# Optimization experiments

Measured on AMD Instinct MI355X. Metric: run time of the kernel, lower is better.

The kernel has to match this reference:

```python
import jax, jax.numpy as jnp
import numpy as np

B, S, D, H = 4, 1024, 1024, 16
DH = D // H
K_SPARSE = 32
LAMBDA_MAX, ALPHA = 10.0, 5.0
SPARSE_THRESHOLD = 1.0


def setup_inputs() -> dict:
    key = jax.random.key(0)
    ks = jax.random.split(key, 12)
    x = jax.random.normal(ks[0], (B, S, D), dtype=jnp.float32)
    prior_mask = jax.random.bernoulli(ks[1], 0.1, (S, S))
    prior_indices = jax.random.randint(ks[2], (S, K_SPARSE), 0, S)
    prior_index_mask = jax.random.bernoulli(ks[3], 0.9, (S, K_SPARSE))
    prior_index_mask = prior_index_mask.at[:, 0].set(True)  # avoid all-masked rows
    u_prev = jax.random.normal(ks[4], (B, 1), dtype=jnp.float32)
    sc = 1.0 / np.sqrt(D)
    Wq = jax.random.normal(ks[5], (D, D), dtype=jnp.float32) * sc
    Wk = jax.random.normal(ks[6], (D, D), dtype=jnp.float32) * sc
    Wv = jax.random.normal(ks[7], (D, D), dtype=jnp.float32) * sc
    Wo = jax.random.normal(ks[8], (D, D), dtype=jnp.float32) * sc
    bq = jnp.zeros((D,), jnp.float32)
    bk = jnp.zeros((D,), jnp.float32)
    bv = jnp.zeros((D,), jnp.float32)
    bo = jnp.zeros((D,), jnp.float32)
    return {"x": x, "prior_mask": prior_mask, "prior_indices": prior_indices,
            "prior_index_mask": prior_index_mask, "u_prev": u_prev,
            "Wq": Wq, "bq": bq, "Wk": Wk, "bk": bk, "Wv": Wv, "bv": bv,
            "Wo": Wo, "bo": bo}


def reference(x, prior_mask, prior_indices, prior_index_mask, u_prev,
              Wq, bq, Wk, bk, Wv, bv, Wo, bo):
    Bb, Ss, Dd = x.shape
    scale = 1.0 / jnp.sqrt(jnp.asarray(DH, x.dtype))

    def proj(W, b):
        return (x @ W.T + b).reshape(Bb, Ss, H, DH).transpose(0, 2, 1, 3)  # [B,H,S,DH]

    Q, K, V = proj(Wq, bq), proj(Wk, bk), proj(Wv, bv)

    lam = LAMBDA_MAX * jnp.exp(-ALPHA * u_prev.reshape(Bb))  # [B]
    use_sparse = lam >= SPARSE_THRESHOLD                      # [B] bool

    # ---- dense branch: full SDPA with lambda-scaled prior bias ----
    scores = jnp.einsum('bhqd,bhkd->bhqk', Q, K) * scale      # [B,H,S,S]
    prior_bias = jnp.where(prior_mask[:Ss, :Ss], 0.0, -1.0).astype(x.dtype)
    bias = lam[:, None, None, None] * prior_bias[None, None]
    dense_out = jnp.einsum('bhqk,bhkd->bhqd',
                           jax.nn.softmax(scores + bias, axis=-1), V)

    # ---- sparse branch: gather-indexed SDPA over prior_indices ----
    idx = prior_indices[:Ss]                                   # [S,k]
    Kg = K[:, :, idx]                                          # [B,H,S,k,DH]
    Vg = V[:, :, idx]
    s_scores = jnp.einsum('bhsd,bhskd->bhsk', Q, Kg) * scale   # [B,H,S,k]
    s_scores = jnp.where(prior_index_mask[:Ss][None, None], s_scores,
                         jnp.asarray(-jnp.inf, x.dtype))
    sparse_out = jnp.einsum('bhsk,bhskd->bhsd',
                            jax.nn.softmax(s_scores, axis=-1), Vg)

    out = jnp.where(use_sparse[:, None, None, None], sparse_out, dense_out)
    out = out.transpose(0, 2, 1, 3).reshape(Bb, Ss, Dd)
    return out @ Wo.T + bo
```

## Files before the change

kernel.cpp:

```cpp
#include <hip/hip_runtime.h>
#include <hip/hip_bf16.h>
#include <cmath>

#define NB 4
#define NS 1024
#define ND 1024
#define NH 16
#define NDH 64
#define NKSP 32
#define SCALE 0.125f

typedef __attribute__((ext_vector_type(8))) short bf16x8;
typedef __attribute__((ext_vector_type(4))) float f32x4;
typedef unsigned long long u64;

#define AS1 __attribute__((address_space(1)))
#define AS3 __attribute__((address_space(3)))

__device__ __forceinline__ void gl_lds16(const void* g, void* l) {
    __builtin_amdgcn_global_load_lds((const AS1 void*)g, (AS3 void*)l, 16, 0, 0);
}

__device__ __forceinline__ ushort f2bf(float f) {
    union { __hip_bfloat16 h; ushort u; } cv;
    cv.h = __float2bfloat16(f);
    return cv.u;
}
__device__ __forceinline__ float bf2f(ushort u) {
    union { unsigned int i; float f; } cv;
    cv.i = ((unsigned int)u) << 16;
    return cv.f;
}

__global__ __launch_bounds__(256)
void f2bf_multi(const float* __restrict__ x,
                const float* __restrict__ w0, const float* __restrict__ w1,
                const float* __restrict__ w2, const float* __restrict__ w3,
                const int* __restrict__ pm,
                ushort* __restrict__ xo,
                ushort* __restrict__ o0, ushort* __restrict__ o1,
                ushort* __restrict__ o2, ushort* __restrict__ o3,
                u64* __restrict__ bm)
{
    int y = blockIdx.y;
    if (y == 5) {
        int word = blockIdx.x * 4 + (threadIdx.x >> 6);
        int lane = threadIdx.x & 63;
        int row  = word >> 4, wcol = word & 15;
        int v = pm[(size_t)row * NS + wcol * 64 + lane];
        u64 b = __ballot(v != 0);
        if (lane == 0) bm[word] = b;
        return;
    }
    const float* src; ushort* dst; int nblk;
    if (y == 0)      { src = x;  dst = xo; nblk = 4096; }
    else if (y == 1) { src = w0; dst = o0; nblk = 1024; }
    else if (y == 2) { src = w1; dst = o1; nblk = 1024; }
    else if (y == 3) { src = w2; dst = o2; nblk = 1024; }
    else             { src = w3; dst = o3; nblk = 1024; }
    if (blockIdx.x >= (unsigned)nblk) return;
    int i = (blockIdx.x * 256 + threadIdx.x) * 4;
    float4 v = *(const float4*)&src[i];
    ushort4 o;
    o.x = f2bf(v.x); o.y = f2bf(v.y); o.z = f2bf(v.z); o.w = f2bf(v.w);
    *(ushort4*)&dst[i] = o;
}

__global__ __launch_bounds__(256)
void gemm_qkv(const ushort* __restrict__ xb,
              const ushort* __restrict__ Wqb, const ushort* __restrict__ Wkb,
              const ushort* __restrict__ Wvb,
              const float* __restrict__ bq, const float* __restrict__ bk,
              const float* __restrict__ bv,
              ushort* __restrict__ Qo, ushort* __restrict__ Ko,
              ushort* __restrict__ Vo, ushort* __restrict__ Vto)
{
    constexpr int K = ND;
    __shared__ __attribute__((aligned(16))) ushort As[128 * 32];
    __shared__ __attribute__((aligned(16))) ushort Bs[128 * 32];

    const int tid  = threadIdx.x;
    const int lane = tid & 63, w = tid >> 6;
    const int wm = w >> 1, wn = w & 1;
    const int which = blockIdx.x >> 3;
    const int n0 = (blockIdx.x & 7) * 128;
    const int m0 = blockIdx.y * 128;
    const int quad = lane >> 4, l16 = lane & 15;

    const ushort* W = (which == 0) ? Wqb : (which == 1) ? Wkb : Wvb;
    const float* bias = (which == 0) ? bq : (which == 1) ? bk : bv;
    ushort* Out = (which == 0) ? Qo : (which == 1) ? Ko : Vo;

    f32x4 acc[4][4] = {};

    for (int k0 = 0; k0 < K; k0 += 32) {
        __syncthreads();
#pragma unroll
        for (int u = 0; u < 2; ++u) {
            int t0 = u * 256 + w * 64;
            int t  = t0 + lane;
            int row = t >> 2, kc = (t & 3) * 8;
            gl_lds16(xb + (size_t)(m0 + row) * K + k0 + kc, &As[t0 * 8]);
            gl_lds16(W  + (size_t)(n0 + row) * K + k0 + kc, &Bs[t0 * 8]);
        }
        __syncthreads();

        bf16x8 af[4], bfr[4];
#pragma unroll
        for (int mt = 0; mt < 4; ++mt)
            af[mt] = *(const bf16x8*)&As[(wm*64 + mt*16 + l16) * 32 + quad*8];
#pragma unroll
        for (int nt = 0; nt < 4; ++nt)
            bfr[nt] = *(const bf16x8*)&Bs[(wn*64 + nt*16 + l16) * 32 + quad*8];
#pragma unroll
        for (int mt = 0; mt < 4; ++mt)
#pragma unroll
            for (int nt = 0; nt < 4; ++nt)
                acc[mt][nt] = __builtin_amdgcn_mfma_f32_16x16x32_bf16(
                    af[mt], bfr[nt], acc[mt][nt], 0, 0, 0);
    }

#pragma unroll
    for (int nt = 0; nt < 4; ++nt) {
        int n = n0 + wn*64 + nt*16 + l16;
        float bz = bias[n];
        int hh = n >> 6, dh = n & 63;
#pragma unroll
        for (int mt = 0; mt < 4; ++mt) {
#pragma unroll
            for (int rg = 0; rg < 4; ++rg) {
                int m = m0 + wm*64 + mt*16 + quad*4 + rg;
                int b = m >> 10, s = m & (NS - 1);
                ushort val = f2bf(acc[mt][nt][rg] + bz);
                Out[(((size_t)(b*NH + hh))*NS + s)*NDH + dh] = val;
                if (which == 2)
                    Vto[(((size_t)(b*NH + hh))*NDH + dh)*NS + s] = val;
            }
        }
    }
}

__global__ __launch_bounds__(256)
void gemm_out(const ushort* __restrict__ A, const ushort* __restrict__ W,
              const float* __restrict__ bias, float* __restrict__ Cout)
{
    constexpr int K = ND;
    __shared__ __attribute__((aligned(16))) ushort As[64 * 32];
    __shared__ __attribute__((aligned(16))) ushort Bs[128 * 32];

    const int tid  = threadIdx.x;
    const int lane = tid & 63, w = tid >> 6;
    const int wm = w & 1, wn = w >> 1;
    const int m0 = blockIdx.y * 64, n0 = blockIdx.x * 128;
    const int quad = lane >> 4, l16 = lane & 15;

    f32x4 acc[2][4] = {};

    for (int k0 = 0; k0 < K; k0 += 32) {
        __syncthreads();
        {
            int t0 = w * 64;
            int t  = t0 + lane;
            int row = t >> 2, kc = (t & 3) * 8;
            gl_lds16(A + (size_t)(m0 + row) * K + k0 + kc, &As[t0 * 8]);
        }
#pragma unroll
        for (int u = 0; u < 2; ++u) {
            int t0 = u * 256 + w * 64;
            int t  = t0 + lane;
            int row = t >> 2, kc = (t & 3) * 8;
            gl_lds16(W + (size_t)(n0 + row) * K + k0 + kc, &Bs[t0 * 8]);
        }
        __syncthreads();

        bf16x8 af[2], bfr[4];
#pragma unroll
        for (int mt = 0; mt < 2; ++mt)
            af[mt] = *(const bf16x8*)&As[(wm*32 + mt*16 + l16) * 32 + quad*8];
#pragma unroll
        for (int nt = 0; nt < 4; ++nt)
            bfr[nt] = *(const bf16x8*)&Bs[(wn*64 + nt*16 + l16) * 32 + quad*8];
#pragma unroll
        for (int mt = 0; mt < 2; ++mt)
#pragma unroll
            for (int nt = 0; nt < 4; ++nt)
                acc[mt][nt] = __builtin_amdgcn_mfma_f32_16x16x32_bf16(
                    af[mt], bfr[nt], acc[mt][nt], 0, 0, 0);
    }

#pragma unroll
    for (int nt = 0; nt < 4; ++nt) {
        int n = n0 + wn*64 + nt*16 + l16;
        float bz = bias[n];
#pragma unroll
        for (int mt = 0; mt < 2; ++mt) {
#pragma unroll
            for (int rg = 0; rg < 4; ++rg) {
                int m = m0 + wm*32 + mt*16 + quad*4 + rg;
                Cout[(size_t)m * ND + n] = acc[mt][nt][rg] + bz;
            }
        }
    }
}

__global__ __launch_bounds__(256)
void attn_kernel(const ushort* __restrict__ Qb, const ushort* __restrict__ Kb,
                 const ushort* __restrict__ Vb, const ushort* __restrict__ Vt,
                 const u64* __restrict__ bm,
                 const int* __restrict__ pidx, const int* __restrict__ pimask,
                 const float* __restrict__ u_prev, ushort* __restrict__ OA)
{
    __shared__ __attribute__((aligned(16))) ushort Ks[64 * 72];
    __shared__ __attribute__((aligned(16))) ushort Vts[64 * 72];
    __shared__ __attribute__((aligned(16))) ushort Ps[128 * 68];
    __shared__ __attribute__((aligned(16))) u64    MW[128 * 16];

    const int tid  = threadIdx.x;
    const int lane = tid & 63, w = tid >> 6;
    const int quad = lane >> 4, l16 = lane & 15;

    const int id    = blockIdx.x;
    const int xcd   = id & 7;
    const int seq   = id >> 3;
    const int head  = xcd * 8 + (seq >> 3);
    const int qtile = seq & 7;
    const int b = head >> 4, h = head & 15;
    const int s0 = qtile * 128;

    const float lam = 10.0f * __expf(-5.0f * u_prev[b]);
    const bool sparse = (lam >= 1.0f);

    const size_t bh = (size_t)b * NH + h;
    const ushort* Qh  = Qb + bh * NS * NDH;
    const ushort* Kh  = Kb + bh * NS * NDH;
    const ushort* Vh  = Vb + bh * NS * NDH;
    const ushort* Vth = Vt + bh * NDH * NS;

    if (!sparse) {
#pragma unroll
        for (int u = 0; u < 8; ++u) {
            int idx = u * 256 + tid;
            MW[idx] = bm[(size_t)s0 * 16 + idx];
        }

        bf16x8 qf[2][2];
#pragma unroll
        for (int qh = 0; qh < 2; ++qh)
#pragma unroll
            for (int kk = 0; kk < 2; ++kk)
                qf[qh][kk] = *(const bf16x8*)
                    &Qh[(size_t)(s0 + w*32 + qh*16 + l16) * NDH + kk*32 + quad*8];

        union { bf16x8 v; ushort s[8]; } ones;
#pragma unroll
        for (int i = 0; i < 8; ++i) ones.s[i] = 0x3F80;

        f32x4 o_acc[2][4] = {};
        f32x4 l_acc[2] = {};

        const int sl = tid >> 2, c0 = (tid & 3) * 16;

        bf16x8 kreg[2], vreg[2];
        {
            const ushort* ksrc = &Kh[(size_t)sl * NDH + c0];
            kreg[0] = *(const bf16x8*)ksrc;
            kreg[1] = *(const bf16x8*)(ksrc + 8);
            const ushort* vsrc = &Vth[(size_t)sl * NS + c0];
            vreg[0] = *(const bf16x8*)vsrc;
            vreg[1] = *(const bf16x8*)(vsrc + 8);
        }

        for (int kt = 0; kt < 16; ++kt) {
            __syncthreads();
            *(bf16x8*)&Ks[sl*72 + c0]      = kreg[0];
            *(bf16x8*)&Ks[sl*72 + c0 + 8]  = kreg[1];
            *(bf16x8*)&Vts[sl*72 + c0]     = vreg[0];
            *(bf16x8*)&Vts[sl*72 + c0 + 8] = vreg[1];
            __syncthreads();

            if (kt < 15) {
                const ushort* ksrc = &Kh[(size_t)((kt+1)*64 + sl) * NDH + c0];
                kreg[0] = *(const bf16x8*)ksrc;
                kreg[1] = *(const bf16x8*)(ksrc + 8);
                const ushort* vsrc = &Vth[(size_t)sl * NS + (kt+1)*64 + c0];
                vreg[0] = *(const bf16x8*)vsrc;
                vreg[1] = *(const bf16x8*)(vsrc + 8);
            }

#pragma unroll
            for (int qh = 0; qh < 2; ++qh) {
                f32x4 s_acc[4] = {};
#pragma unroll
                for (int nt = 0; nt < 4; ++nt)
#pragma unroll
                    for (int kk = 0; kk < 2; ++kk) {
                        bf16x8 kf = *(const bf16x8*)&Ks[(nt*16 + l16)*72 + kk*32 + quad*8];
                        s_acc[nt] = __builtin_amdgcn_mfma_f32_16x16x32_bf16(
                            qf[qh][kk], kf, s_acc[nt], 0, 0, 0);
                    }

                u64 wv[4];
#pragma unroll
                for (int rg = 0; rg < 4; ++rg)
                    wv[rg] = MW[(w*32 + qh*16 + quad*4 + rg) * 16 + kt];
#pragma unroll
                for (int nt = 0; nt < 4; ++nt)
#pragma unroll
                    for (int rg = 0; rg < 4; ++rg) {
                        float bias = ((wv[rg] >> (nt*16 + l16)) & 1ULL) ? 0.f : -lam;
                        float p = __expf(fmaf(s_acc[nt][rg], SCALE, bias));
                        Ps[(w*32 + qh*16 + quad*4 + rg) * 68 + nt*16 + l16] = f2bf(p);
                    }

                bf16x8 pf[2];
#pragma unroll
                for (int kk = 0; kk < 2; ++kk)
                    pf[kk] = *(const bf16x8*)&Ps[(w*32 + qh*16 + l16)*68 + kk*32 + quad*8];
#pragma unroll
                for (int kk = 0; kk < 2; ++kk) {
                    l_acc[qh] = __builtin_amdgcn_mfma_f32_16x16x32_bf16(
                        pf[kk], ones.v, l_acc[qh], 0, 0, 0);
#pragma unroll
                    for (int nt = 0; nt < 4; ++nt) {
                        bf16x8 vf = *(const bf16x8*)&Vts[(nt*16 + l16)*72 + kk*32 + quad*8];
                        o_acc[qh][nt] = __builtin_amdgcn_mfma_f32_16x16x32_bf16(
                            pf[kk], vf, o_acc[qh][nt], 0, 0, 0);
                    }
                }
            }
        }

#pragma unroll
        for (int qh = 0; qh < 2; ++qh) {
            float inv[4];
#pragma unroll
            for (int rg = 0; rg < 4; ++rg) inv[rg] = 1.f / l_acc[qh][rg];
#pragma unroll
            for (int nt = 0; nt < 4; ++nt)
#pragma unroll
                for (int rg = 0; rg < 4; ++rg) {
                    int m = w*32 + qh*16 + quad*4 + rg;
                    OA[((size_t)b*NS + s0 + m)*ND + h*NDH + nt*16 + l16] =
                        f2bf(o_acc[qh][nt][rg] * inv[rg]);
                }
        }
    } else {
        const int r   = lane & 15;
        const int cg  = lane >> 4;
#pragma unroll
        for (int qh = 0; qh < 2; ++qh) {
            const int row = w*32 + qh*16 + r;

            float qreg[64];
            {
                const ushort* qp = Qh + (size_t)(s0 + row) * NDH;
#pragma unroll
                for (int c = 0; c < 8; ++c) {
                    union { bf16x8 v; ushort s[8]; } qv;
                    qv.v = *(const bf16x8*)(qp + c*8);
#pragma unroll
                    for (int j = 0; j < 8; ++j) qreg[c*8 + j] = bf2f(qv.s[j]);
                }
            }

            float sc[8];
#pragma unroll
            for (int jj = 0; jj < 8; ++jj) {
                int j  = cg*8 + jj;
                int mv = pimask[(size_t)(s0+row)*NKSP + j];
                if (mv) {
                    int kv = pidx[(size_t)(s0+row)*NKSP + j];
                    const ushort* krow = &Kh[(size_t)kv * NDH];
                    float acc = 0.f;
#pragma unroll
                    for (int c = 0; c < 8; ++c) {
                        union { bf16x8 v; ushort s[8]; } kk;
                        kk.v = *(const bf16x8*)(krow + c*8);
#pragma unroll
                        for (int jb = 0; jb < 8; ++jb)
                            acc = fmaf(qreg[c*8 + jb], bf2f(kk.s[jb]), acc);
                    }
                    sc[jj] = acc * SCALE;
                } else {
                    sc[jj] = -INFINITY;
                }
            }
            float mt = sc[0];
#pragma unroll
            for (int jj = 1; jj < 8; ++jj) mt = fmaxf(mt, sc[jj]);
            mt = fmaxf(mt, __shfl_xor(mt, 16));
            mt = fmaxf(mt, __shfl_xor(mt, 32));

            float psum = 0.f;
#pragma unroll
            for (int jj = 0; jj < 8; ++jj) {
                float p = __expf(sc[jj] - mt);
                psum += p;
                Ps[row * 68 + cg*8 + jj] = f2bf(p);
            }
            psum += __shfl_xor(psum, 16);
            psum += __shfl_xor(psum, 32);

            float o[16];
#pragma unroll
            for (int i = 0; i < 16; ++i) o[i] = 0.f;

            for (int j = 0; j < 32; ++j) {
                float p = bf2f(Ps[row * 68 + j]);
                if (p != 0.f) {
                    int kv = pidx[(size_t)(s0+row)*NKSP + j];
                    const ushort* vrow = &Vh[(size_t)kv * NDH + cg*16];
#pragma unroll
                    for (int c = 0; c < 2; ++c) {
                        union { bf16x8 v; ushort s[8]; } vv;
                        vv.v = *(const bf16x8*)(vrow + c*8);
#pragma unroll
                        for (int jb = 0; jb < 8; ++jb)
                            o[c*8 + jb] = fmaf(p, bf2f(vv.s[jb]), o[c*8 + jb]);
                    }
                }
            }

            float inv = 1.f / psum;
            ushort* op = OA + ((size_t)b*NS + s0 + row)*ND + h*NDH + cg*16;
#pragma unroll
            for (int i4 = 0; i4 < 4; ++i4) {
                ushort4 v;
                v.x = f2bf(o[i4*4+0]*inv); v.y = f2bf(o[i4*4+1]*inv);
                v.z = f2bf(o[i4*4+2]*inv); v.w = f2bf(o[i4*4+3]*inv);
                *(ushort4*)(op + i4*4) = v;
            }
        }
    }
}

extern "C" void kernel_launch(void* const* d_in, const int* in_sizes, int n_in,
                              void* d_out, int out_size, void* d_ws, size_t ws_size,
                              hipStream_t stream)
{
    const float* x      = (const float*)d_in[0];
    const int*   pmask  = (const int*)  d_in[1];
    const int*   pidx   = (const int*)  d_in[2];
    const int*   pimask = (const int*)  d_in[3];
    const float* u_prev = (const float*)d_in[4];
    const float* Wq     = (const float*)d_in[5];
    const float* bq     = (const float*)d_in[6];
    const float* Wk     = (const float*)d_in[7];
    const float* bk     = (const float*)d_in[8];
    const float* Wv     = (const float*)d_in[9];
    const float* bv     = (const float*)d_in[10];
    const float* Wo     = (const float*)d_in[11];
    const float* bo     = (const float*)d_in[12];
    float* out = (float*)d_out;

    const size_t QSZ = (size_t)NB * NH * NS * NDH;
    const size_t WSZ = (size_t)ND * ND;
    ushort* xb  = (ushort*)d_ws;
    ushort* Qw  = xb  + QSZ;
    ushort* Kw  = Qw  + QSZ;
    ushort* Vw  = Kw  + QSZ;
    ushort* Vtw = Vw  + QSZ;
    ushort* Awb = Vtw + QSZ;
    ushort* Wqb = Awb + QSZ;
    ushort* Wkb = Wqb + WSZ;
    ushort* Wvb = Wkb + WSZ;
    ushort* Wob = Wvb + WSZ;
    u64*    bmw = (u64*)(Wob + WSZ);

    f2bf_multi<<<dim3(4096, 6), 256, 0, stream>>>(
        x, Wq, Wk, Wv, Wo, pmask, xb, Wqb, Wkb, Wvb, Wob, bmw);

    gemm_qkv<<<dim3(24, 32), 256, 0, stream>>>(
        xb, Wqb, Wkb, Wvb, bq, bk, bv, Qw, Kw, Vw, Vtw);

    attn_kernel<<<512, 256, 0, stream>>>(
        Qw, Kw, Vw, Vtw, bmw, pidx, pimask, u_prev, Awb);

    gemm_out<<<dim3(ND/128, (NB*NS)/64), 256, 0, stream>>>(Awb, Wob, bo, out);
}
```

Measured before the change: 238.7 us.

## Stage QKV epilogue through LDS and double-buffer K/V tiles in attention

The QKV GEMM epilogue now writes results into an LDS tile, then stores Q/K/V rows as 16-byte vectors and builds the transposed V through LDS, replacing scattered 2-byte global stores. The attention kernel double-buffers its K and V LDS tiles so the next tile is written after compute, removing one barrier per iteration. It also preloads all K/V fragments into registers and pads the P buffer stride to 72. A launch bound of two blocks per SIMD is added, which may limit registers now that more fragments are held live.

```diff
diff --git a/kernel.cpp b/kernel.cpp
--- a/kernel.cpp
+++ b/kernel.cpp
@@ -78,6 +78,7 @@
     constexpr int K = ND;
     __shared__ __attribute__((aligned(16))) ushort As[128 * 32];
     __shared__ __attribute__((aligned(16))) ushort Bs[128 * 32];
+    __shared__ __attribute__((aligned(16))) ushort Cs[128 * 72];
 
     const int tid  = threadIdx.x;
     const int lane = tid & 63, w = tid >> 6;
@@ -120,22 +121,45 @@
                     af[mt], bfr[nt], acc[mt][nt], 0, 0, 0);
     }
 
-#pragma unroll
-    for (int nt = 0; nt < 4; ++nt) {
-        int n = n0 + wn*64 + nt*16 + l16;
-        float bz = bias[n];
-        int hh = n >> 6, dh = n & 63;
-#pragma unroll
-        for (int mt = 0; mt < 4; ++mt) {
-#pragma unroll
-            for (int rg = 0; rg < 4; ++rg) {
-                int m = m0 + wm*64 + mt*16 + quad*4 + rg;
-                int b = m >> 10, s = m & (NS - 1);
-                ushort val = f2bf(acc[mt][nt][rg] + bz);
-                Out[(((size_t)(b*NH + hh))*NS + s)*NDH + dh] = val;
-                if (which == 2)
-                    Vto[(((size_t)(b*NH + hh))*NDH + dh)*NS + s] = val;
-            }
+    const int b = m0 >> 10, sbase = m0 & (NS - 1);
+
+#pragma unroll
+    for (int p = 0; p < 2; ++p) {
+        __syncthreads();
+        if (wn == p) {
+#pragma unroll
+            for (int nt = 0; nt < 4; ++nt) {
+                int ncol = nt*16 + l16;
+                float bz = bias[n0 + p*64 + ncol];
+#pragma unroll
+                for (int mt = 0; mt < 4; ++mt)
+#pragma unroll
+                    for (int rg = 0; rg < 4; ++rg) {
+                        int m = wm*64 + mt*16 + quad*4 + rg;
+                        Cs[m*72 + ncol] = f2bf(acc[mt][nt][rg] + bz);
+                    }
+            }
+        }
+        __syncthreads();
+
+        int hh = (n0 >> 6) + p;
+        {
+            int r = tid >> 1, cc = (tid & 1) * 32;
+            const ushort* csp = &Cs[r*72 + cc];
+            ushort* gp = Out + (((size_t)(b*NH + hh))*NS + sbase + r)*NDH + cc;
+#pragma unroll
+            for (int j = 0; j < 4; ++j)
+                *(bf16x8*)(gp + j*8) = *(const bf16x8*)(csp + j*8);
+        }
+        if (which == 2) {
+            int dh = tid >> 2, sc2 = (tid & 3) * 32;
+            ushort tmp[32];
+#pragma unroll
+            for (int i = 0; i < 32; ++i) tmp[i] = Cs[(sc2 + i)*72 + dh];
+            ushort* vp = Vto + (((size_t)(b*NH + hh))*NDH + dh)*NS + sbase + sc2;
+#pragma unroll
+            for (int j = 0; j < 4; ++j)
+                *(bf16x8*)(vp + j*8) = *(bf16x8*)&tmp[j*8];
         }
     }
 }
@@ -203,16 +227,16 @@
     }
 }
 
-__global__ __launch_bounds__(256)
+__global__ __launch_bounds__(256, 2)
 void attn_kernel(const ushort* __restrict__ Qb, const ushort* __restrict__ Kb,
                  const ushort* __restrict__ Vb, const ushort* __restrict__ Vt,
                  const u64* __restrict__ bm,
                  const int* __restrict__ pidx, const int* __restrict__ pimask,
                  const float* __restrict__ u_prev, ushort* __restrict__ OA)
 {
-    __shared__ __attribute__((aligned(16))) ushort Ks[64 * 72];
-    __shared__ __attribute__((aligned(16))) ushort Vts[64 * 72];
-    __shared__ __attribute__((aligned(16))) ushort Ps[128 * 68];
+    __shared__ __attribute__((aligned(16))) ushort Ks[2][64 * 72];
+    __shared__ __attribute__((aligned(16))) ushort Vts[2][64 * 72];
+    __shared__ __attribute__((aligned(16))) ushort Ps[128 * 72];
     __shared__ __attribute__((aligned(16))) u64    MW[128 * 16];
 
     const int tid  = threadIdx.x;
@@ -269,14 +293,14 @@
             vreg[0] = *(const bf16x8*)vsrc;
             vreg[1] = *(const bf16x8*)(vsrc + 8);
         }
+        *(bf16x8*)&Ks[0][sl*72 + c0]      = kreg[0];
+        *(bf16x8*)&Ks[0][sl*72 + c0 + 8]  = kreg[1];
+        *(bf16x8*)&Vts[0][sl*72 + c0]     = vreg[0];
+        *(bf16x8*)&Vts[0][sl*72 + c0 + 8] = vreg[1];
+        __syncthreads();
 
         for (int kt = 0; kt < 16; ++kt) {
-            __syncthreads();
-            *(bf16x8*)&Ks[sl*72 + c0]      = kreg[0];
-            *(bf16x8*)&Ks[sl*72 + c0 + 8]  = kreg[1];
-            *(bf16x8*)&Vts[sl*72 + c0]     = vreg[0];
-            *(bf16x8*)&Vts[sl*72 + c0 + 8] = vreg[1];
-            __syncthreads();
+            const int cur = kt & 1;
 
             if (kt < 15) {
                 const ushort* ksrc = &Kh[(size_t)((kt+1)*64 + sl) * NDH + c0];
@@ -287,17 +311,24 @@
                 vreg[1] = *(const bf16x8*)(vsrc + 8);
             }
 
+            bf16x8 kf[4][2], vf[4][2];
+#pragma unroll
+            for (int nt = 0; nt < 4; ++nt)
+#pragma unroll
+                for (int kk = 0; kk < 2; ++kk) {
+                    kf[nt][kk] = *(const bf16x8*)&Ks[cur][(nt*16 + l16)*72 + kk*32 + quad*8];
+                    vf[nt][kk] = *(const bf16x8*)&Vts[cur][(nt*16 + l16)*72 + kk*32 + quad*8];
+                }
+
 #pragma unroll
             for (int qh = 0; qh < 2; ++qh) {
                 f32x4 s_acc[4] = {};
 #pragma unroll
                 for (int nt = 0; nt < 4; ++nt)
 #pragma unroll
-                    for (int kk = 0; kk < 2; ++kk) {
-                        bf16x8 kf = *(const bf16x8*)&Ks[(nt*16 + l16)*72 + kk*32 + quad*8];
+                    for (int kk = 0; kk < 2; ++kk)
                         s_acc[nt] = __builtin_amdgcn_mfma_f32_16x16x32_bf16(
-                            qf[qh][kk], kf, s_acc[nt], 0, 0, 0);
-                    }
+                            qf[qh][kk], kf[nt][kk], s_acc[nt], 0, 0, 0);
 
                 u64 wv[4];
 #pragma unroll
@@ -309,25 +340,32 @@
                     for (int rg = 0; rg < 4; ++rg) {
                         float bias = ((wv[rg] >> (nt*16 + l16)) & 1ULL) ? 0.f : -lam;
                         float p = __expf(fmaf(s_acc[nt][rg], SCALE, bias));
-                        Ps[(w*32 + qh*16 + quad*4 + rg) * 68 + nt*16 + l16] = f2bf(p);
+                        Ps[(w*32 + qh*16 + quad*4 + rg) * 72 + nt*16 + l16] = f2bf(p);
                     }
 
                 bf16x8 pf[2];
 #pragma unroll
                 for (int kk = 0; kk < 2; ++kk)
-                    pf[kk] = *(const bf16x8*)&Ps[(w*32 + qh*16 + l16)*68 + kk*32 + quad*8];
+                    pf[kk] = *(const bf16x8*)&Ps[(w*32 + qh*16 + l16)*72 + kk*32 + quad*8];
 #pragma unroll
                 for (int kk = 0; kk < 2; ++kk) {
                     l_acc[qh] = __builtin_amdgcn_mfma_f32_16x16x32_bf16(
                         pf[kk], ones.v, l_acc[qh], 0, 0, 0);
 #pragma unroll
-                    for (int nt = 0; nt < 4; ++nt) {
-                        bf16x8 vf = *(const bf16x8*)&Vts[(nt*16 + l16)*72 + kk*32 + quad*8];
+                    for (int nt = 0; nt < 4; ++nt)
                         o_acc[qh][nt] = __builtin_amdgcn_mfma_f32_16x16x32_bf16(
-                            pf[kk], vf, o_acc[qh][nt], 0, 0, 0);
-                    }
+                            pf[kk], vf[nt][kk], o_acc[qh][nt], 0, 0, 0);
                 }
             }
+
+            if (kt < 15) {
+                const int nxt = cur ^ 1;
+                *(bf16x8*)&Ks[nxt][sl*72 + c0]      = kreg[0];
+                *(bf16x8*)&Ks[nxt][sl*72 + c0 + 8]  = kreg[1];
+                *(bf16x8*)&Vts[nxt][sl*72 + c0]     = vreg[0];
+                *(bf16x8*)&Vts[nxt][sl*72 + c0 + 8] = vreg[1];
+            }
+            __syncthreads();
         }
 
 #pragma unroll
@@ -396,7 +434,7 @@
             for (int jj = 0; jj < 8; ++jj) {
                 float p = __expf(sc[jj] - mt);
                 psum += p;
-                Ps[row * 68 + cg*8 + jj] = f2bf(p);
+                Ps[row * 72 + cg*8 + jj] = f2bf(p);
             }
             psum += __shfl_xor(psum, 16);
             psum += __shfl_xor(psum, 32);
@@ -406,7 +444,7 @@
             for (int i = 0; i < 16; ++i) o[i] = 0.f;
 
             for (int j = 0; j < 32; ++j) {
-                float p = bf2f(Ps[row * 68 + j]);
+                float p = bf2f(Ps[row * 72 + j]);
                 if (p != 0.f) {
                     int kv = pidx[(size_t)(s0+row)*NKSP + j];
                     const ushort* vrow = &Vh[(size_t)kv * NDH + cg*16];
```

New measurement: 253.1 us. 6.0% more time.

## Split dense attention over two KV halves with atomic accumulation and normalize pass

Applied to the files above, without the earlier changes.

Each head/query tile is split across two blocks, each covering half the key range, doubling the grid to 1024 blocks for better occupancy. Partial unnormalized outputs and row sums are atomically added into the output buffer (used as scratch) and a row-sum buffer, and a new kernel normalizes and converts to bf16. The K/V fragments are also hoisted into registers once per tile. This adds two memsets, fp32 atomics traffic and an extra kernel launch. It relies on there being no running-max subtraction in the dense path.

```diff
diff --git a/kernel.cpp b/kernel.cpp
--- a/kernel.cpp
+++ b/kernel.cpp
@@ -204,16 +204,18 @@
 }
 
 __global__ __launch_bounds__(256)
-void attn_kernel(const ushort* __restrict__ Qb, const ushort* __restrict__ Kb,
-                 const ushort* __restrict__ Vb, const ushort* __restrict__ Vt,
-                 const u64* __restrict__ bm,
-                 const int* __restrict__ pidx, const int* __restrict__ pimask,
-                 const float* __restrict__ u_prev, ushort* __restrict__ OA)
+void attn_split(const ushort* __restrict__ Qb, const ushort* __restrict__ Kb,
+                const ushort* __restrict__ Vb, const ushort* __restrict__ Vt,
+                const u64* __restrict__ bm,
+                const int* __restrict__ pidx, const int* __restrict__ pimask,
+                const float* __restrict__ u_prev,
+                float* __restrict__ Od, float* __restrict__ Lb,
+                ushort* __restrict__ OA)
 {
     __shared__ __attribute__((aligned(16))) ushort Ks[64 * 72];
     __shared__ __attribute__((aligned(16))) ushort Vts[64 * 72];
-    __shared__ __attribute__((aligned(16))) ushort Ps[128 * 68];
-    __shared__ __attribute__((aligned(16))) u64    MW[128 * 16];
+    __shared__ __attribute__((aligned(16))) ushort Ps[128 * 72];
+    __shared__ __attribute__((aligned(16))) u64    MW[128 * 8];
 
     const int tid  = threadIdx.x;
     const int lane = tid & 63, w = tid >> 6;
@@ -221,9 +223,11 @@
 
     const int id    = blockIdx.x;
     const int xcd   = id & 7;
-    const int seq   = id >> 3;
-    const int head  = xcd * 8 + (seq >> 3);
-    const int qtile = seq & 7;
+    const int r     = id >> 3;
+    const int head  = (r >> 4) * 8 + xcd;
+    const int rem   = r & 15;
+    const int qtile = rem >> 1;
+    const int sp    = rem & 1;
     const int b = head >> 4, h = head & 15;
     const int s0 = qtile * 128;
 
@@ -237,10 +241,11 @@
     const ushort* Vth = Vt + bh * NDH * NS;
 
     if (!sparse) {
-#pragma unroll
-        for (int u = 0; u < 8; ++u) {
+        const int kt0 = sp * 8;
+#pragma unroll
+        for (int u = 0; u < 4; ++u) {
             int idx = u * 256 + tid;
-            MW[idx] = bm[(size_t)s0 * 16 + idx];
+            MW[idx] = bm[(size_t)(s0 + (idx >> 3)) * 16 + kt0 + (idx & 7)];
         }
 
         bf16x8 qf[2][2];
@@ -262,15 +267,16 @@
 
         bf16x8 kreg[2], vreg[2];
         {
-            const ushort* ksrc = &Kh[(size_t)sl * NDH + c0];
+            const ushort* ksrc = &Kh[(size_t)(kt0*64 + sl) * NDH + c0];
             kreg[0] = *(const bf16x8*)ksrc;
             kreg[1] = *(const bf16x8*)(ksrc + 8);
-            const ushort* vsrc = &Vth[(size_t)sl * NS + c0];
+            const ushort* vsrc = &Vth[(size_t)sl * NS + kt0*64 + c0];
             vreg[0] = *(const bf16x8*)vsrc;
             vreg[1] = *(const bf16x8*)(vsrc + 8);
         }
 
-        for (int kt = 0; kt < 16; ++kt) {
+        for (int t = 0; t < 8; ++t) {
+            const int kt = kt0 + t;
             __syncthreads();
             *(bf16x8*)&Ks[sl*72 + c0]      = kreg[0];
             *(bf16x8*)&Ks[sl*72 + c0 + 8]  = kreg[1];
@@ -278,7 +284,7 @@
             *(bf16x8*)&Vts[sl*72 + c0 + 8] = vreg[1];
             __syncthreads();
 
-            if (kt < 15) {
+            if (t < 7) {
                 const ushort* ksrc = &Kh[(size_t)((kt+1)*64 + sl) * NDH + c0];
                 kreg[0] = *(const bf16x8*)ksrc;
                 kreg[1] = *(const bf16x8*)(ksrc + 8);
@@ -287,69 +293,79 @@
                 vreg[1] = *(const bf16x8*)(vsrc + 8);
             }
 
+            bf16x8 kf[4][2], vf[4][2];
+#pragma unroll
+            for (int nt = 0; nt < 4; ++nt)
+#pragma unroll
+                for (int kk = 0; kk < 2; ++kk) {
+                    kf[nt][kk] = *(const bf16x8*)&Ks[(nt*16 + l16)*72 + kk*32 + quad*8];
+                    vf[nt][kk] = *(const bf16x8*)&Vts[(nt*16 + l16)*72 + kk*32 + quad*8];
+                }
+
 #pragma unroll
             for (int qh = 0; qh < 2; ++qh) {
                 f32x4 s_acc[4] = {};
 #pragma unroll
                 for (int nt = 0; nt < 4; ++nt)
 #pragma unroll
-                    for (int kk = 0; kk < 2; ++kk) {
-                        bf16x8 kf = *(const bf16x8*)&Ks[(nt*16 + l16)*72 + kk*32 + quad*8];
+                    for (int kk = 0; kk < 2; ++kk)
                         s_acc[nt] = __builtin_amdgcn_mfma_f32_16x16x32_bf16(
-                            qf[qh][kk], kf, s_acc[nt], 0, 0, 0);
-                    }
+                            qf[qh][kk], kf[nt][kk], s_acc[nt], 0, 0, 0);
 
                 u64 wv[4];
 #pragma unroll
                 for (int rg = 0; rg < 4; ++rg)
-                    wv[rg] = MW[(w*32 + qh*16 + quad*4 + rg) * 16 + kt];
+                    wv[rg] = MW[(w*32 + qh*16 + quad*4 + rg) * 8 + t];
 #pragma unroll
                 for (int nt = 0; nt < 4; ++nt)
 #pragma unroll
                     for (int rg = 0; rg < 4; ++rg) {
                         float bias = ((wv[rg] >> (nt*16 + l16)) & 1ULL) ? 0.f : -lam;
                         float p = __expf(fmaf(s_acc[nt][rg], SCALE, bias));
-                        Ps[(w*32 + qh*16 + quad*4 + rg) * 68 + nt*16 + l16] = f2bf(p);
+                        Ps[(w*32 + qh*16 + quad*4 + rg) * 72 + nt*16 + l16] = f2bf(p);
                     }
 
                 bf16x8 pf[2];
 #pragma unroll
                 for (int kk = 0; kk < 2; ++kk)
-                    pf[kk] = *(const bf16x8*)&Ps[(w*32 + qh*16 + l16)*68 + kk*32 + quad*8];
+                    pf[kk] = *(const bf16x8*)&Ps[(w*32 + qh*16 + l16)*72 + kk*32 + quad*8];
 #pragma unroll
                 for (int kk = 0; kk < 2; ++kk) {
                     l_acc[qh] = __builtin_amdgcn_mfma_f32_16x16x32_bf16(
                         pf[kk], ones.v, l_acc[qh], 0, 0, 0);
 #pragma unroll
-                    for (int nt = 0; nt < 4; ++nt) {
-                        bf16x8 vf = *(const bf16x8*)&Vts[(nt*16 + l16)*72 + kk*32 + quad*8];
+                    for (int nt = 0; nt < 4; ++nt)
                         o_acc[qh][nt] = __builtin_amdgcn_mfma_f32_16x16x32_bf16(
-                            pf[kk], vf, o_acc[qh][nt], 0, 0, 0);
-                    }
+                            pf[kk], vf[nt][kk], o_acc[qh][nt], 0, 0, 0);
                 }
             }
         }
 
 #pragma unroll
         for (int qh = 0; qh < 2; ++qh) {
-            float inv[4];
-#pragma unroll
-            for (int rg = 0; rg < 4; ++rg) inv[rg] = 1.f / l_acc[qh][rg];
 #pragma unroll
             for (int nt = 0; nt < 4; ++nt)
 #pragma unroll
                 for (int rg = 0; rg < 4; ++rg) {
                     int m = w*32 + qh*16 + quad*4 + rg;
-                    OA[((size_t)b*NS + s0 + m)*ND + h*NDH + nt*16 + l16] =
-                        f2bf(o_acc[qh][nt][rg] * inv[rg]);
-                }
+                    atomicAdd(&Od[((size_t)b*NS + s0 + m)*ND + h*NDH + nt*16 + l16],
+                              o_acc[qh][nt][rg]);
+                }
+            if (l16 == 0) {
+#pragma unroll
+                for (int rg = 0; rg < 4; ++rg) {
+                    int m = w*32 + qh*16 + quad*4 + rg;
+                    atomicAdd(&Lb[bh*NS + s0 + m], l_acc[qh][rg]);
+                }
+            }
         }
     } else {
-        const int r   = lane & 15;
+        if (sp) return;
+        const int r2  = lane & 15;
         const int cg  = lane >> 4;
 #pragma unroll
         for (int qh = 0; qh < 2; ++qh) {
-            const int row = w*32 + qh*16 + r;
+            const int row = w*32 + qh*16 + r2;
 
             float qreg[64];
             {
@@ -396,7 +412,7 @@
             for (int jj = 0; jj < 8; ++jj) {
                 float p = __expf(sc[jj] - mt);
                 psum += p;
-                Ps[row * 68 + cg*8 + jj] = f2bf(p);
+                Ps[row * 72 + cg*8 + jj] = f2bf(p);
             }
             psum += __shfl_xor(psum, 16);
             psum += __shfl_xor(psum, 32);
@@ -406,7 +422,7 @@
             for (int i = 0; i < 16; ++i) o[i] = 0.f;
 
             for (int j = 0; j < 32; ++j) {
-                float p = bf2f(Ps[row * 68 + j]);
+                float p = bf2f(Ps[row * 72 + j]);
                 if (p != 0.f) {
                     int kv = pidx[(size_t)(s0+row)*NKSP + j];
                     const ushort* vrow = &Vh[(size_t)kv * NDH + cg*16];
@@ -432,6 +448,24 @@
             }
         }
     }
+}
+
+__global__ __launch_bounds__(256)
+void norm_attn(const float* __restrict__ Od, const float* __restrict__ Lb,
+               const float* __restrict__ u_prev, ushort* __restrict__ OA)
+{
+    int bs = blockIdx.x;
+    int b = bs >> 10, s = bs & (NS - 1);
+    float lam = 10.0f * __expf(-5.0f * u_prev[b]);
+    if (lam >= 1.0f) return;
+    int c = threadIdx.x * 4;
+    int h = c >> 6;
+    float inv = 1.f / Lb[((size_t)b*NH + h)*NS + s];
+    float4 v = *(const float4*)&Od[((size_t)b*NS + s)*ND + c];
+    ushort4 o;
+    o.x = f2bf(v.x*inv); o.y = f2bf(v.y*inv);
+    o.z = f2bf(v.z*inv); o.w = f2bf(v.w*inv);
+    *(ushort4*)&OA[((size_t)b*NS + s)*ND + c] = o;
 }
 
 extern "C" void kernel_launch(void* const* d_in, const int* in_sizes, int n_in,
@@ -466,6 +500,10 @@
     ushort* Wvb = Wkb + WSZ;
     ushort* Wob = Wvb + WSZ;
     u64*    bmw = (u64*)(Wob + WSZ);
+    float*  Lb  = (float*)(bmw + NS*16);
+
+    hipMemsetAsync(d_out, 0, (size_t)out_size * sizeof(float), stream);
+    hipMemsetAsync(Lb, 0, (size_t)NB * NH * NS * sizeof(float), stream);
 
     f2bf_multi<<<dim3(4096, 6), 256, 0, stream>>>(
         x, Wq, Wk, Wv, Wo, pmask, xb, Wqb, Wkb, Wvb, Wob, bmw);
@@ -473,8 +511,10 @@
     gemm_qkv<<<dim3(24, 32), 256, 0, stream>>>(
         xb, Wqb, Wkb, Wvb, bq, bk, bv, Qw, Kw, Vw, Vtw);
 
-    attn_kernel<<<512, 256, 0, stream>>>(
-        Qw, Kw, Vw, Vtw, bmw, pidx, pimask, u_prev, Awb);
+    attn_split<<<1024, 256, 0, stream>>>(
+        Qw, Kw, Vw, Vtw, bmw, pidx, pimask, u_prev, (float*)d_out, Lb, Awb);
+
+    norm_attn<<<4096, 256, 0, stream>>>((const float*)d_out, Lb, u_prev, Awb);
 
     gemm_out<<<dim3(ND/128, (NB*NS)/64), 256, 0, stream>>>(Awb, Wob, bo, out);
 }
```

Measured after the change: 299.5 us. +25.5%, slower.

## Swap MFMA operands to transpose S, hoist K/V fragments, vectorize P stores

Applied to the files above, without the earlier changes.

In the dense attention path the QK^T MFMA now takes K as the A operand and Q as B. Each lane therefore holds four consecutive key columns for one query row, so the mask needs one 64-bit word per lane and P is written to LDS as a packed ushort4 instead of 16 scalar stores. K and V fragments are loaded from LDS once per key tile and reused across both query halves, at the cost of more registers. The block-to-head mapping is changed so that neighbouring heads spread across XCDs, and the Ps row stride becomes 72.

```diff
diff --git a/kernel.cpp b/kernel.cpp
--- a/kernel.cpp
+++ b/kernel.cpp
@@ -212,7 +212,7 @@
 {
     __shared__ __attribute__((aligned(16))) ushort Ks[64 * 72];
     __shared__ __attribute__((aligned(16))) ushort Vts[64 * 72];
-    __shared__ __attribute__((aligned(16))) ushort Ps[128 * 68];
+    __shared__ __attribute__((aligned(16))) ushort Ps[128 * 72];
     __shared__ __attribute__((aligned(16))) u64    MW[128 * 16];
 
     const int tid  = threadIdx.x;
@@ -221,9 +221,9 @@
 
     const int id    = blockIdx.x;
     const int xcd   = id & 7;
-    const int seq   = id >> 3;
-    const int head  = xcd * 8 + (seq >> 3);
-    const int qtile = seq & 7;
+    const int t5    = id >> 3;
+    const int qtile = t5 & 7;
+    const int head  = (t5 >> 3) * 8 + xcd;
     const int b = head >> 4, h = head & 15;
     const int s0 = qtile * 128;
 
@@ -287,45 +287,57 @@
                 vreg[1] = *(const bf16x8*)(vsrc + 8);
             }
 
+            bf16x8 kf[4][2], vf[4][2];
+#pragma unroll
+            for (int nt = 0; nt < 4; ++nt)
+#pragma unroll
+                for (int kk = 0; kk < 2; ++kk) {
+                    kf[nt][kk] = *(const bf16x8*)&Ks[(nt*16 + l16)*72 + kk*32 + quad*8];
+                    vf[nt][kk] = *(const bf16x8*)&Vts[(nt*16 + l16)*72 + kk*32 + quad*8];
+                }
+
 #pragma unroll
             for (int qh = 0; qh < 2; ++qh) {
+                const int qrow = w*32 + qh*16 + l16;
+
                 f32x4 s_acc[4] = {};
 #pragma unroll
                 for (int nt = 0; nt < 4; ++nt)
 #pragma unroll
-                    for (int kk = 0; kk < 2; ++kk) {
-                        bf16x8 kf = *(const bf16x8*)&Ks[(nt*16 + l16)*72 + kk*32 + quad*8];
+                    for (int kk = 0; kk < 2; ++kk)
                         s_acc[nt] = __builtin_amdgcn_mfma_f32_16x16x32_bf16(
-                            qf[qh][kk], kf, s_acc[nt], 0, 0, 0);
-                    }
-
-                u64 wv[4];
-#pragma unroll
-                for (int rg = 0; rg < 4; ++rg)
-                    wv[rg] = MW[(w*32 + qh*16 + quad*4 + rg) * 16 + kt];
-#pragma unroll
-                for (int nt = 0; nt < 4; ++nt)
-#pragma unroll
-                    for (int rg = 0; rg < 4; ++rg) {
-                        float bias = ((wv[rg] >> (nt*16 + l16)) & 1ULL) ? 0.f : -lam;
-                        float p = __expf(fmaf(s_acc[nt][rg], SCALE, bias));
-                        Ps[(w*32 + qh*16 + quad*4 + rg) * 68 + nt*16 + l16] = f2bf(p);
-                    }
+                            kf[nt][kk], qf[qh][kk], s_acc[nt], 0, 0, 0);
+
+                u64 wq = MW[qrow * 16 + kt] >> (quad * 4);
+#pragma unroll
+                for (int nt = 0; nt < 4; ++nt) {
+                    ushort4 pk;
+                    float p0, p1, p2, p3;
+                    p0 = __expf(fmaf(s_acc[nt][0], SCALE,
+                         ((wq >> (nt*16 + 0)) & 1ULL) ? 0.f : -lam));
+                    p1 = __expf(fmaf(s_acc[nt][1], SCALE,
+                         ((wq >> (nt*16 + 1)) & 1ULL) ? 0.f : -lam));
+                    p2 = __expf(fmaf(s_acc[nt][2], SCALE,
+                         ((wq >> (nt*16 + 2)) & 1ULL) ? 0.f : -lam));
+                    p3 = __expf(fmaf(s_acc[nt][3], SCALE,
+                         ((wq >> (nt*16 + 3)) & 1ULL) ? 0.f : -lam));
+                    pk.x = f2bf(p0); pk.y = f2bf(p1);
+                    pk.z = f2bf(p2); pk.w = f2bf(p3);
+                    *(ushort4*)&Ps[qrow*72 + nt*16 + quad*4] = pk;
+                }
 
                 bf16x8 pf[2];
 #pragma unroll
                 for (int kk = 0; kk < 2; ++kk)
-                    pf[kk] = *(const bf16x8*)&Ps[(w*32 + qh*16 + l16)*68 + kk*32 + quad*8];
+                    pf[kk] = *(const bf16x8*)&Ps[qrow*72 + kk*32 + quad*8];
 #pragma unroll
                 for (int kk = 0; kk < 2; ++kk) {
                     l_acc[qh] = __builtin_amdgcn_mfma_f32_16x16x32_bf16(
                         pf[kk], ones.v, l_acc[qh], 0, 0, 0);
 #pragma unroll
-                    for (int nt = 0; nt < 4; ++nt) {
-                        bf16x8 vf = *(const bf16x8*)&Vts[(nt*16 + l16)*72 + kk*32 + quad*8];
+                    for (int nt = 0; nt < 4; ++nt)
                         o_acc[qh][nt] = __builtin_amdgcn_mfma_f32_16x16x32_bf16(
-                            pf[kk], vf, o_acc[qh][nt], 0, 0, 0);
-                    }
+                            pf[kk], vf[nt][kk], o_acc[qh][nt], 0, 0, 0);
                 }
             }
         }
@@ -345,11 +357,11 @@
                 }
         }
     } else {
-        const int r   = lane & 15;
+        const int r2  = lane & 15;
         const int cg  = lane >> 4;
 #pragma unroll
         for (int qh = 0; qh < 2; ++qh) {
-            const int row = w*32 + qh*16 + r;
+            const int row = w*32 + qh*16 + r2;
 
             float qreg[64];
             {
@@ -396,7 +408,7 @@
             for (int jj = 0; jj < 8; ++jj) {
                 float p = __expf(sc[jj] - mt);
                 psum += p;
-                Ps[row * 68 + cg*8 + jj] = f2bf(p);
+                Ps[row * 72 + cg*8 + jj] = f2bf(p);
             }
             psum += __shfl_xor(psum, 16);
             psum += __shfl_xor(psum, 32);
@@ -406,7 +418,7 @@
             for (int i = 0; i < 16; ++i) o[i] = 0.f;
 
             for (int j = 0; j < 32; ++j) {
-                float p = bf2f(Ps[row * 68 + j]);
+                float p = bf2f(Ps[row * 72 + j]);
                 if (p != 0.f) {
                     int kv = pidx[(size_t)(s0+row)*NKSP + j];
                     const ushort* vrow = &Vh[(size_t)kv * NDH + cg*16];
```

Result: no change. 237.3 us (-0.6%).
